# Optimization experiments

Measured on AMD Instinct MI355X. Metric: run time of the kernel, lower is better.

The kernel has to match this reference:

```python
import jax, jax.numpy as jnp
import numpy as np

LN_EPS = 1e-12


def setup_inputs() -> dict:
    key = jax.random.key(0)
    ks = jax.random.split(key, 10)
    B, S, W, D, H = 16, 512, 5, 200, 768
    std = 0.02
    return {
        "layer_output": jax.random.normal(ks[0], (B, S, H), dtype=jnp.float32),
        "word_embeddings": jax.random.normal(ks[1], (B, S, W, D), dtype=jnp.float32),
        "word_mask": jax.random.randint(ks[2], (B, S, W), 0, 2, dtype=jnp.int64),
        "W1": jax.random.normal(ks[3], (D, H), dtype=jnp.float32) * std,
        "b1": jnp.zeros((H,), dtype=jnp.float32),
        "W2": jax.random.normal(ks[4], (H, H), dtype=jnp.float32) * std,
        "b2": jnp.zeros((H,), dtype=jnp.float32),
        "attn_W": jax.random.normal(ks[5], (H, H), dtype=jnp.float32) * std,
        "ln_gamma": jnp.ones((H,), dtype=jnp.float32),
        "ln_beta": jnp.zeros((H,), dtype=jnp.float32),
    }


def reference(layer_output, word_embeddings, word_mask, W1, b1, W2, b2, attn_W, ln_gamma, ln_beta):
    # word_transform: Linear -> Tanh -> Linear (dropout = identity in eval)
    we = jnp.tanh(jnp.einsum("bswd,dh->bswh", word_embeddings, W1) + b1)
    we = jnp.einsum("bswh,hk->bswk", we, W2) + b2  # [B,S,W,H]

    # bilinear word attention: (x @ attn_W) . word_outputs -> score over W
    q = jnp.einsum("bsh,hk->bsk", layer_output, attn_W)  # [B,S,H]
    alpha = jnp.einsum("bsk,bswk->bsw", q, we)            # [B,S,W]
    alpha = alpha + (1.0 - word_mask.astype(alpha.dtype)) * -10000.0
    alpha = jax.nn.softmax(alpha, axis=-1)

    # weighted sum over words + residual
    agg = jnp.einsum("bsw,bswh->bsh", alpha, we)
    h = layer_output + agg

    # LayerNorm (fuse_layer; dropout = identity in eval)
    mu = jnp.mean(h, axis=-1, keepdims=True)
    var = jnp.mean(jnp.square(h - mu), axis=-1, keepdims=True)
    return (h - mu) * jax.lax.rsqrt(var + LN_EPS) * ln_gamma + ln_beta
```

## Files before the change

kernel.cpp:

```cpp
#include <hip/hip_runtime.h>
#include <hip/hip_bf16.h>
#include <math.h>


typedef __attribute__((ext_vector_type(8))) short bf16x8;
typedef __attribute__((ext_vector_type(4))) float f32x4;

__device__ __forceinline__ unsigned short f2bf_bits(float f) {
    __hip_bfloat16 h = __float2bfloat16(f);
    return *reinterpret_cast<unsigned short*>(&h);
}
__device__ __forceinline__ float bf_bits2f(unsigned short u) {
    union { unsigned int i; float f; } v; v.i = ((unsigned int)u) << 16; return v.f;
}
__device__ __forceinline__ float tanh_fast(float x) {
    float xc = fminf(fmaxf(x, -9.f), 9.f);
    float t  = __expf(2.f * xc);
    return (t - 1.f) * __builtin_amdgcn_rcpf(t + 1.f);
}
__device__ __forceinline__ bf16x8 pack8(float4 a, float4 b) {
    union { bf16x8 v; unsigned short s[8]; } u;
    u.s[0]=f2bf_bits(a.x); u.s[1]=f2bf_bits(a.y); u.s[2]=f2bf_bits(a.z); u.s[3]=f2bf_bits(a.w);
    u.s[4]=f2bf_bits(b.x); u.s[5]=f2bf_bits(b.y); u.s[6]=f2bf_bits(b.z); u.s[7]=f2bf_bits(b.w);
    return u.v;
}

__device__ __forceinline__ void async_cp16(const void* g, void* lds) {
#if __has_builtin(__builtin_amdgcn_global_load_lds)
    auto gp = (const __attribute__((address_space(1))) unsigned int*)g;
    auto lp = (__attribute__((address_space(3))) unsigned int*)lds;
    __builtin_amdgcn_global_load_lds(gp, lp, 16, 0, 0);
#else
    *(uint4*)lds = *(const uint4*)g;
#endif
}

__device__ __forceinline__ void sched_fence()  { asm volatile("" ::: "memory"); }
__device__ __forceinline__ void wait8_barrier(){ asm volatile("s_waitcnt vmcnt(8)\ns_barrier" ::: "memory"); }
__device__ __forceinline__ void wait0_barrier(){ asm volatile("s_waitcnt vmcnt(0)\ns_barrier" ::: "memory"); }
__device__ __forceinline__ void barrier_only() { asm volatile("s_barrier" ::: "memory"); }

template<bool F32SRC, bool SINGLE, bool HAS_BIAS, bool TANH_ACT, bool RESID, bool OUT_BF16,
         int N, int K, int KREAL>
__device__ __forceinline__ void gemm_body(
    const void* __restrict__ Ap, const void* __restrict__ Btp,
    const float* __restrict__ bias, const float* __restrict__ resid,
    void* __restrict__ outp, int m0, int n0, unsigned char* smem)
{
    constexpr int NIT = K / 64;
    const int tid  = threadIdx.x;
    const int lane = tid & 63;
    const int wave = tid >> 6;
    const int wm   = wave & 1;
    const int wn   = wave >> 1;
    const int row16 = lane & 15;
    const int kq    = lane >> 4;

    f32x4 acc[4][4];
#pragma unroll
    for (int i = 0; i < 4; i++)
#pragma unroll
        for (int j = 0; j < 4; j++) acc[i][j] = (f32x4){0.f, 0.f, 0.f, 0.f};

    auto compute_tile = [&](const unsigned short* As, const unsigned short* Bs, bool full) {
        bf16x8 af[2][4], bg[2][4];
#pragma unroll
        for (int mi = 0; mi < 4; mi++) {
            const int r = wm * 64 + mi * 16 + row16;
            af[0][mi] = *(const bf16x8*)&As[r * 64 + (kq ^ (r & 7)) * 8];
            if (full) af[1][mi] = *(const bf16x8*)&As[r * 64 + ((4 + kq) ^ (r & 7)) * 8];
        }
#pragma unroll
        for (int ni = 0; ni < 4; ni++) {
            const int r = wn * 64 + ni * 16 + row16;
            bg[0][ni] = *(const bf16x8*)&Bs[r * 64 + (kq ^ (r & 7)) * 8];
            if (full) bg[1][ni] = *(const bf16x8*)&Bs[r * 64 + ((4 + kq) ^ (r & 7)) * 8];
        }
        __builtin_amdgcn_s_setprio(1);
#pragma unroll
        for (int mi = 0; mi < 4; mi++)
#pragma unroll
            for (int ni = 0; ni < 4; ni++)
                acc[mi][ni] = __builtin_amdgcn_mfma_f32_16x16x32_bf16(
                    af[0][mi], bg[0][ni], acc[mi][ni], 0, 0, 0);
        if (full) {
#pragma unroll
            for (int mi = 0; mi < 4; mi++)
#pragma unroll
                for (int ni = 0; ni < 4; ni++)
                    acc[mi][ni] = __builtin_amdgcn_mfma_f32_16x16x32_bf16(
                        af[1][mi], bg[1][ni], acc[mi][ni], 0, 0, 0);
        }
        __builtin_amdgcn_s_setprio(0);
    };

    if constexpr (F32SRC) {
        const float* A32 = (const float*)Ap;
        const float* B32 = (const float*)Btp;
        unsigned short* As = (unsigned short*)smem;
        unsigned short* Bs = As + 8192;
        for (int t = 0; t < NIT; ++t) {
#pragma unroll
            for (int i = 0; i < 4; ++i) {
                const int c = i * 256 + tid;
                const int row = c >> 3, sl = c & 7;
                const int kcc = sl ^ (row & 7);
                const float* sa = A32 + (size_t)(m0 + row) * K + t * 64 + kcc * 8;
                *(bf16x8*)&As[row * 64 + sl * 8] = pack8(*(const float4*)sa, *(const float4*)(sa + 4));
                const float* sb = B32 + (size_t)(n0 + row) * K + t * 64 + kcc * 8;
                *(bf16x8*)&Bs[row * 64 + sl * 8] = pack8(*(const float4*)sb, *(const float4*)(sb + 4));
            }
            __syncthreads();
            compute_tile(As, Bs, true);
            __syncthreads();
        }
    } else {
        const __hip_bfloat16* A  = (const __hip_bfloat16*)Ap;
        const __hip_bfloat16* Bt = (const __hip_bfloat16*)Btp;
        const int rsub = lane >> 3;
        const int slot = lane & 7;
        const int kc   = slot ^ rsub;
        const __hip_bfloat16* gA = A  + (size_t)(m0 + wave * 32 + rsub) * K + kc * 8;
        const __hip_bfloat16* gB = Bt + (size_t)(n0 + wave * 32 + rsub) * K + kc * 8;
        unsigned short* lA0 = (unsigned short*)smem + wave * 2048 + lane * 8;
        unsigned short* lB0 = lA0 + 8192;

        auto stage = [&](int t, int buf) {
            unsigned short* lA = lA0 + buf * 16384;
            unsigned short* lB = lB0 + buf * 16384;
            const __hip_bfloat16* a = gA + t * 64;
            const __hip_bfloat16* b = gB + t * 64;
#pragma unroll
            for (int i = 0; i < 4; i++) {
                async_cp16(a + (size_t)(8 * i) * K, lA + i * 512);
                async_cp16(b + (size_t)(8 * i) * K, lB + i * 512);
            }
            sched_fence();
        };

        if constexpr (SINGLE) {
            static_assert(!SINGLE || NIT <= 4, "SINGLE path needs K<=256 (128KB LDS)");
#pragma unroll
            for (int t = 0; t < NIT; ++t) stage(t, t);
            wait0_barrier();
#pragma unroll
            for (int t = 0; t < NIT; ++t) {
                const unsigned short* As = (const unsigned short*)(smem + t * 32768);
                compute_tile(As, As + 8192, (t * 64 + 32 < KREAL));
            }
            barrier_only();
        } else {
            stage(0, 0);
            if (NIT > 1) stage(1, 1);
#pragma unroll
            for (int t = 0; t < NIT; ++t) {
                if (t == NIT - 1) wait0_barrier(); else wait8_barrier();
                const unsigned short* As = (const unsigned short*)(smem + (t & 1) * 32768);
                const unsigned short* Bs = As + 8192;
                compute_tile(As, Bs, (t * 64 + 32 < KREAL));
                barrier_only();
                if (t + 2 < NIT) stage(t + 2, t & 1);
            }
        }
    }

    if (OUT_BF16) {
        unsigned short* rep = (unsigned short*)smem;
#pragma unroll
        for (int ni = 0; ni < 4; ni++) {
            const int c = wn * 64 + ni * 16 + row16;
            float bcol = HAS_BIAS ? bias[n0 + c] : 0.f;
#pragma unroll
            for (int mi = 0; mi < 4; mi++)
#pragma unroll
                for (int r = 0; r < 4; r++) {
                    const int rr = wm * 64 + mi * 16 + kq * 4 + r;
                    float v = acc[mi][ni][r];
                    if (HAS_BIAS) v += bcol;
                    if (TANH_ACT) v = tanh_fast(v);
                    rep[rr * 132 + c] = f2bf_bits(v);
                }
        }
        __syncthreads();
#pragma unroll
        for (int p = 0; p < 8; p++) {
            const int lin = p * 256 + tid;
            const int row = lin >> 4;
            const int c8  = lin & 15;
            const unsigned short* s = &rep[row * 132 + c8 * 8];
            union { uint4 u; unsigned long long q[2]; } d;
            d.q[0] = *(const unsigned long long*)(s);
            d.q[1] = *(const unsigned long long*)(s + 4);
            *(uint4*)((__hip_bfloat16*)outp + (size_t)(m0 + row) * N + n0 + c8 * 8) = d.u;
        }
    } else {
        float* rep = (float*)smem;
#pragma unroll
        for (int h = 0; h < 2; h++) {
            if (wm == h) {
#pragma unroll
                for (int ni = 0; ni < 4; ni++) {
                    const int c = wn * 64 + ni * 16 + row16;
                    float bcol = HAS_BIAS ? bias[n0 + c] : 0.f;
#pragma unroll
                    for (int mi = 0; mi < 4; mi++)
#pragma unroll
                        for (int r = 0; r < 4; r++) {
                            const int rr = mi * 16 + kq * 4 + r;
                            float v = acc[mi][ni][r];
                            if (HAS_BIAS) v += bcol;
                            if (TANH_ACT) v = tanh_fast(v);
                            rep[rr * 132 + c] = v;
                        }
                }
            }
            __syncthreads();
#pragma unroll
            for (int p = 0; p < 8; p++) {
                const int lin = p * 256 + tid;
                const int row = lin >> 5;
                const int c4  = lin & 31;
                float4 v = *(const float4*)&rep[row * 132 + c4 * 4];
                const int grow = m0 + h * 64 + row;
                if (RESID) {
                    float4 rv = *(const float4*)&resid[(size_t)grow * N + n0 + c4 * 4];
                    v.x += rv.x; v.y += rv.y; v.z += rv.z; v.w += rv.w;
                }
                *(float4*)((float*)outp + (size_t)grow * N + n0 + c4 * 4) = v;
            }
            __syncthreads();
        }
    }
}

template<bool HAS_BIAS, bool TANH_ACT, bool RESID, bool OUT_BF16, int N, int K, int GX>
__global__ __launch_bounds__(256) void mfma_gemm(
    const __hip_bfloat16* __restrict__ A,
    const __hip_bfloat16* __restrict__ Bt,
    const float* __restrict__ bias,
    const float* __restrict__ resid,
    void* __restrict__ outp)
{
    __shared__ __align__(16) unsigned char smem[65536];
    int bx, by;
    {
        const int total = gridDim.x;
        const int per_xcd = total >> 3;
        if ((total & 7) == 0 && (per_xcd % GX) == 0) {
            int xcd = blockIdx.x & 7, idx = blockIdx.x >> 3;
            int lin = xcd * per_xcd + idx;
            by = lin / GX; bx = lin % GX;
        } else { by = blockIdx.x / GX; bx = blockIdx.x % GX; }
    }
    gemm_body<false, false, HAS_BIAS, TANH_ACT, RESID, OUT_BF16, N, K, K>(
        A, Bt, bias, resid, outp, by * 128, bx * 128, smem);
}

__global__ __launch_bounds__(256) void tgemm_kernel(
    const __hip_bfloat16* __restrict__ Eb,
    const __hip_bfloat16* __restrict__ W1Tb,
    const float* __restrict__ b1,
    __hip_bfloat16* __restrict__ Tb)
{
    __shared__ __align__(16) unsigned char smem[131072];
    const int xcd = blockIdx.x & 7, idx = blockIdx.x >> 3;
    const int lin = xcd * 240 + idx;
    gemm_body<false, true, true, true, false, true, 768, 256, 224>(
        Eb, W1Tb, b1, nullptr, Tb, (lin / 6) * 128, (lin % 6) * 128, smem);
}

__global__ __launch_bounds__(256) void prep_kernel(
    const float* __restrict__ x,  __hip_bfloat16* __restrict__ xb,
    const float* __restrict__ w2,
    const float* __restrict__ aw,
    const float* __restrict__ E,  __hip_bfloat16* __restrict__ Eb,
    const float* __restrict__ W1, __hip_bfloat16* __restrict__ W1Tb,
    __hip_bfloat16* __restrict__ W2Tb,
    __hip_bfloat16* __restrict__ Ctb)
{
    __shared__ __align__(16) unsigned char smem[33792];
    float (*tile)[33] = (float(*)[33])smem;
    const int b = blockIdx.x, tid = threadIdx.x;
    if (b < 6144) {
        long long i = (long long)b * 256 + tid;
        float4 v = ((const float4*)x)[i];
        ((ushort4*)xb)[i] = make_ushort4(f2bf_bits(v.x), f2bf_bits(v.y), f2bf_bits(v.z), f2bf_bits(v.w));
    } else if (b < 16384) {
        const int lane = tid & 63, wave = tid >> 6;
        const long long row = (long long)(b - 6144) * 4 + wave;
        const int k = lane * 4;
        float4 v = make_float4(0.f, 0.f, 0.f, 0.f);
        if (k < 200) v = *(const float4*)&E[row * 200 + k];
        *(ushort4*)&Eb[row * 256 + k] =
            make_ushort4(f2bf_bits(v.x), f2bf_bits(v.y), f2bf_bits(v.z), f2bf_bits(v.w));
    } else if (b < 17152) {
        const float* in; __hip_bfloat16* outb; int R, C, Rpad, t;
        if (b < 16576) { t = b - 16384; in = W1; outb = W1Tb; R = 200; C = 768; Rpad = 256; }
        else           { t = b - 16576; in = w2; outb = W2Tb; R = 768; C = 768; Rpad = 768; }
        const int c0 = (t % 24) * 32, r0 = (t / 24) * 32;
        const int xx = tid & 31, yy = tid >> 5;
#pragma unroll
        for (int i = 0; i < 32; i += 8) {
            int r = r0 + yy + i;
            tile[yy + i][xx] = (r < R) ? in[(size_t)r * C + c0 + xx] : 0.f;
        }
        __syncthreads();
#pragma unroll
        for (int i = 0; i < 32; i += 8)
            outb[(size_t)(c0 + yy + i) * Rpad + r0 + xx] = __float2bfloat16(tile[xx][yy + i]);
    } else {
        const int id = b - 17152;
        gemm_body<true, false, false, false, false, true, 768, 768, 768>(
            w2, aw, nullptr, nullptr, Ctb, (id / 6) * 128, (id % 6) * 128, smem);
    }
}

__global__ __launch_bounds__(256) void attn_kernel(
    const __hip_bfloat16* __restrict__ T,
    const __hip_bfloat16* P,
    const int* __restrict__ mask,
    __hip_bfloat16* S)
{
    const int lane = threadIdx.x & 63;
    const int wave = threadIdx.x >> 6;
    const int r    = blockIdx.x * 4 + wave;
    const int base = lane * 12;

    float pv[12];
    {
        const ushort4* pp = (const ushort4*)((const unsigned short*)P + (size_t)r * 768 + base);
        ushort4 u0 = pp[0], u1 = pp[1], u2 = pp[2];
        unsigned short us[12] = {u0.x,u0.y,u0.z,u0.w, u1.x,u1.y,u1.z,u1.w, u2.x,u2.y,u2.z,u2.w};
#pragma unroll
        for (int j = 0; j < 12; j++) pv[j] = bf_bits2f(us[j]);
    }
    float tv[5][12], part[5];
#pragma unroll
    for (int w = 0; w < 5; w++) {
        const ushort4* tp = (const ushort4*)((const unsigned short*)T + ((size_t)r * 5 + w) * 768 + base);
        ushort4 u0 = tp[0], u1 = tp[1], u2 = tp[2];
        unsigned short us[12] = {u0.x,u0.y,u0.z,u0.w, u1.x,u1.y,u1.z,u1.w, u2.x,u2.y,u2.z,u2.w};
        float s = 0.f;
#pragma unroll
        for (int j = 0; j < 12; j++) { tv[w][j] = bf_bits2f(us[j]); s += tv[w][j] * pv[j]; }
        part[w] = s;
    }
#pragma unroll
    for (int off = 32; off > 0; off >>= 1)
#pragma unroll
        for (int w = 0; w < 5; w++)
            part[w] += __shfl_xor(part[w], off, 64);

    float logit[5], mx = -1e30f;
#pragma unroll
    for (int w = 0; w < 5; w++) {
        float m = (float)mask[(size_t)r * 5 + w];
        logit[w] = part[w] - 10000.0f * (1.0f - m);
        mx = fmaxf(mx, logit[w]);
    }
    float se = 0.f;
#pragma unroll
    for (int w = 0; w < 5; w++) { logit[w] = expf(logit[w] - mx); se += logit[w]; }
    const float inv = 1.0f / se;

    unsigned short os[12];
#pragma unroll
    for (int j = 0; j < 12; j++) {
        float s = 0.f;
#pragma unroll
        for (int w = 0; w < 5; w++) s += logit[w] * tv[w][j];
        os[j] = f2bf_bits(s * inv);
    }
    ushort4* sp = (ushort4*)((unsigned short*)S + (size_t)r * 768 + base);
    sp[0] = make_ushort4(os[0], os[1], os[2],  os[3]);
    sp[1] = make_ushort4(os[4], os[5], os[6],  os[7]);
    sp[2] = make_ushort4(os[8], os[9], os[10], os[11]);
}

__global__ __launch_bounds__(256) void ln_kernel(
    const float* __restrict__ Hbuf, const float* __restrict__ gamma,
    const float* __restrict__ beta, float* __restrict__ out)
{
    const int lane = threadIdx.x & 63;
    const int wave = threadIdx.x >> 6;
    const int r    = blockIdx.x * 4 + wave;
    const float* hr = Hbuf + (size_t)r * 768 + lane * 12;

    float v[12];
    {
        float4 a = *(const float4*)(hr);
        float4 b = *(const float4*)(hr + 4);
        float4 c = *(const float4*)(hr + 8);
        v[0]=a.x; v[1]=a.y; v[2]=a.z; v[3]=a.w;
        v[4]=b.x; v[5]=b.y; v[6]=b.z; v[7]=b.w;
        v[8]=c.x; v[9]=c.y; v[10]=c.z; v[11]=c.w;
    }
    float s = 0.f;
#pragma unroll
    for (int j = 0; j < 12; j++) s += v[j];
#pragma unroll
    for (int off = 32; off > 0; off >>= 1) s += __shfl_xor(s, off, 64);
    const float mu = s * (1.f / 768.f);
    float vs = 0.f;
#pragma unroll
    for (int j = 0; j < 12; j++) { float d = v[j] - mu; vs += d * d; }
#pragma unroll
    for (int off = 32; off > 0; off >>= 1) vs += __shfl_xor(vs, off, 64);
    const float rs = rsqrtf(vs * (1.f / 768.f) + 1e-12f);

    float o[12];
#pragma unroll
    for (int j = 0; j < 12; j++) {
        int h = lane * 12 + j;
        o[j] = (v[j] - mu) * rs * gamma[h] + beta[h];
    }
    float* orow = out + (size_t)r * 768 + lane * 12;
    *(float4*)(orow)     = make_float4(o[0], o[1], o[2],  o[3]);
    *(float4*)(orow + 4) = make_float4(o[4], o[5], o[6],  o[7]);
    *(float4*)(orow + 8) = make_float4(o[8], o[9], o[10], o[11]);
}

extern "C" void kernel_launch(void* const* d_in, const int* in_sizes, int n_in,
                              void* d_out, int out_size, void* d_ws, size_t ws_size,
                              hipStream_t stream)
{
    const float* x      = (const float*)d_in[0];
    const float* E      = (const float*)d_in[1];
    const int*   mask   = (const int*)d_in[2];
    const float* W1     = (const float*)d_in[3];
    const float* b1     = (const float*)d_in[4];
    const float* W2     = (const float*)d_in[5];
    const float* b2     = (const float*)d_in[6];
    const float* attn_W = (const float*)d_in[7];
    const float* gamma  = (const float*)d_in[8];
    const float* beta   = (const float*)d_in[9];
    float* out = (float*)d_out;

    const int BS = 8192, H = 768, M1 = 40960, KP = 256;

    char* p = (char*)d_ws;
    auto alloc = [&](size_t bytes) { char* q = p; p += (bytes + 255) & ~(size_t)255; return q; };
    __hip_bfloat16* xb    = (__hip_bfloat16*)alloc((size_t)BS * H * 2);
    __hip_bfloat16* W2Tb  = (__hip_bfloat16*)alloc((size_t)H * H * 2);
    __hip_bfloat16* Ctb   = (__hip_bfloat16*)alloc((size_t)H * H * 2);
    __hip_bfloat16* W1Tb  = (__hip_bfloat16*)alloc((size_t)H * KP * 2);
    __hip_bfloat16* Tb    = (__hip_bfloat16*)alloc((size_t)M1 * H * 2);
    __hip_bfloat16* Eb    = (__hip_bfloat16*)alloc((size_t)M1 * KP * 2);
    float* Hb = (float*)Tb;
    __hip_bfloat16* Pb = Eb;
    __hip_bfloat16* Sb = Pb;

    prep_kernel<<<17188, 256, 0, stream>>>(x, xb, W2, attn_W, E, Eb, W1, W1Tb, W2Tb, Ctb);

    tgemm_kernel<<<1920, 256, 0, stream>>>(Eb, W1Tb, b1, Tb);

    mfma_gemm<false, false, false, true, 768, 768, 6><<<384, 256, 0, stream>>>(
        xb, Ctb, nullptr, nullptr, Pb);

    attn_kernel<<<BS / 4, 256, 0, stream>>>(Tb, Pb, mask, Sb);

    mfma_gemm<true, false, true, false, 768, 768, 6><<<384, 256, 0, stream>>>(
        Sb, W2Tb, b2, x, Hb);

    ln_kernel<<<BS / 4, 256, 0, stream>>>(Hb, gamma, beta, out);
}
```

Baseline: 252.0 us.

## Double-buffer tgemm with 64KB LDS and coarsen prep kernel blocks

The first GEMM drops its single-shot load of all four K tiles into 128KB of LDS and uses the same two-buffer pipelined loop as the other GEMMs, with 64KB LDS. This is meant to allow higher occupancy and overlap loads with MFMA work. The prep kernel moves its long Ctb GEMM blocks to the front of the grid so they start early. Each conversion block now handles 8x more float4 or row work, which cuts the grid from 17188 to 2852 blocks and lowers per-block overhead, at the cost of less parallelism per block.

```diff
diff --git a/kernel.cpp b/kernel.cpp
--- a/kernel.cpp
+++ b/kernel.cpp
@@ -40,7 +40,7 @@
 __device__ __forceinline__ void wait0_barrier(){ asm volatile("s_waitcnt vmcnt(0)\ns_barrier" ::: "memory"); }
 __device__ __forceinline__ void barrier_only() { asm volatile("s_barrier" ::: "memory"); }
 
-template<bool F32SRC, bool SINGLE, bool HAS_BIAS, bool TANH_ACT, bool RESID, bool OUT_BF16,
+template<bool F32SRC, bool HAS_BIAS, bool TANH_ACT, bool RESID, bool OUT_BF16,
          int N, int K, int KREAL>
 __device__ __forceinline__ void gemm_body(
     const void* __restrict__ Ap, const void* __restrict__ Btp,
@@ -138,29 +138,16 @@
             sched_fence();
         };
 
-        if constexpr (SINGLE) {
-            static_assert(!SINGLE || NIT <= 4, "SINGLE path needs K<=256 (128KB LDS)");
-#pragma unroll
-            for (int t = 0; t < NIT; ++t) stage(t, t);
-            wait0_barrier();
-#pragma unroll
-            for (int t = 0; t < NIT; ++t) {
-                const unsigned short* As = (const unsigned short*)(smem + t * 32768);
-                compute_tile(As, As + 8192, (t * 64 + 32 < KREAL));
-            }
+        stage(0, 0);
+        if (NIT > 1) stage(1, 1);
+#pragma unroll
+        for (int t = 0; t < NIT; ++t) {
+            if (t == NIT - 1) wait0_barrier(); else wait8_barrier();
+            const unsigned short* As = (const unsigned short*)(smem + (t & 1) * 32768);
+            const unsigned short* Bs = As + 8192;
+            compute_tile(As, Bs, (t * 64 + 32 < KREAL));
             barrier_only();
-        } else {
-            stage(0, 0);
-            if (NIT > 1) stage(1, 1);
-#pragma unroll
-            for (int t = 0; t < NIT; ++t) {
-                if (t == NIT - 1) wait0_barrier(); else wait8_barrier();
-                const unsigned short* As = (const unsigned short*)(smem + (t & 1) * 32768);
-                const unsigned short* Bs = As + 8192;
-                compute_tile(As, Bs, (t * 64 + 32 < KREAL));
-                barrier_only();
-                if (t + 2 < NIT) stage(t + 2, t & 1);
-            }
+            if (t + 2 < NIT) stage(t + 2, t & 1);
         }
     }
 
@@ -252,7 +239,7 @@
             by = lin / GX; bx = lin % GX;
         } else { by = blockIdx.x / GX; bx = blockIdx.x % GX; }
     }
-    gemm_body<false, false, HAS_BIAS, TANH_ACT, RESID, OUT_BF16, N, K, K>(
+    gemm_body<false, HAS_BIAS, TANH_ACT, RESID, OUT_BF16, N, K, K>(
         A, Bt, bias, resid, outp, by * 128, bx * 128, smem);
 }
 
@@ -262,10 +249,10 @@
     const float* __restrict__ b1,
     __hip_bfloat16* __restrict__ Tb)
 {
-    __shared__ __align__(16) unsigned char smem[131072];
+    __shared__ __align__(16) unsigned char smem[65536];
     const int xcd = blockIdx.x & 7, idx = blockIdx.x >> 3;
     const int lin = xcd * 240 + idx;
-    gemm_body<false, true, true, true, false, true, 768, 256, 224>(
+    gemm_body<false, true, true, false, true, 768, 256, 224>(
         Eb, W1Tb, b1, nullptr, Tb, (lin / 6) * 128, (lin % 6) * 128, smem);
 }
 
@@ -281,22 +268,13 @@
     __shared__ __align__(16) unsigned char smem[33792];
     float (*tile)[33] = (float(*)[33])smem;
     const int b = blockIdx.x, tid = threadIdx.x;
-    if (b < 6144) {
-        long long i = (long long)b * 256 + tid;
-        float4 v = ((const float4*)x)[i];
-        ((ushort4*)xb)[i] = make_ushort4(f2bf_bits(v.x), f2bf_bits(v.y), f2bf_bits(v.z), f2bf_bits(v.w));
-    } else if (b < 16384) {
-        const int lane = tid & 63, wave = tid >> 6;
-        const long long row = (long long)(b - 6144) * 4 + wave;
-        const int k = lane * 4;
-        float4 v = make_float4(0.f, 0.f, 0.f, 0.f);
-        if (k < 200) v = *(const float4*)&E[row * 200 + k];
-        *(ushort4*)&Eb[row * 256 + k] =
-            make_ushort4(f2bf_bits(v.x), f2bf_bits(v.y), f2bf_bits(v.z), f2bf_bits(v.w));
-    } else if (b < 17152) {
+    if (b < 36) {
+        gemm_body<true, false, false, false, true, 768, 768, 768>(
+            w2, aw, nullptr, nullptr, Ctb, (b / 6) * 128, (b % 6) * 128, smem);
+    } else if (b < 804) {
         const float* in; __hip_bfloat16* outb; int R, C, Rpad, t;
-        if (b < 16576) { t = b - 16384; in = W1; outb = W1Tb; R = 200; C = 768; Rpad = 256; }
-        else           { t = b - 16576; in = w2; outb = W2Tb; R = 768; C = 768; Rpad = 768; }
+        if (b < 228) { t = b - 36;  in = W1; outb = W1Tb; R = 200; C = 768; Rpad = 256; }
+        else         { t = b - 228; in = w2; outb = W2Tb; R = 768; C = 768; Rpad = 768; }
         const int c0 = (t % 24) * 32, r0 = (t / 24) * 32;
         const int xx = tid & 31, yy = tid >> 5;
 #pragma unroll
@@ -308,10 +286,29 @@
 #pragma unroll
         for (int i = 0; i < 32; i += 8)
             outb[(size_t)(c0 + yy + i) * Rpad + r0 + xx] = __float2bfloat16(tile[xx][yy + i]);
+    } else if (b < 1572) {
+        const long long base = (long long)(b - 804) * 2048 + tid;
+        float4 v[8];
+#pragma unroll
+        for (int j = 0; j < 8; j++) v[j] = ((const float4*)x)[base + j * 256];
+#pragma unroll
+        for (int j = 0; j < 8; j++)
+            ((ushort4*)xb)[base + j * 256] =
+                make_ushort4(f2bf_bits(v[j].x), f2bf_bits(v[j].y), f2bf_bits(v[j].z), f2bf_bits(v[j].w));
     } else {
-        const int id = b - 17152;
-        gemm_body<true, false, false, false, false, true, 768, 768, 768>(
-            w2, aw, nullptr, nullptr, Ctb, (id / 6) * 128, (id % 6) * 128, smem);
+        const int lane = tid & 63, wave = tid >> 6;
+        const long long r0 = (long long)(b - 1572) * 32 + wave * 8;
+        const int k = lane * 4;
+        float4 v[8];
+#pragma unroll
+        for (int j = 0; j < 8; j++) {
+            v[j] = make_float4(0.f, 0.f, 0.f, 0.f);
+            if (k < 200) v[j] = *(const float4*)&E[(r0 + j) * 200 + k];
+        }
+#pragma unroll
+        for (int j = 0; j < 8; j++)
+            *(ushort4*)&Eb[(r0 + j) * 256 + k] =
+                make_ushort4(f2bf_bits(v[j].x), f2bf_bits(v[j].y), f2bf_bits(v[j].z), f2bf_bits(v[j].w));
     }
 }
 
@@ -450,7 +447,7 @@
     __hip_bfloat16* Pb = Eb;
     __hip_bfloat16* Sb = Pb;
 
-    prep_kernel<<<17188, 256, 0, stream>>>(x, xb, W2, attn_W, E, Eb, W1, W1Tb, W2Tb, Ctb);
+    prep_kernel<<<2852, 256, 0, stream>>>(x, xb, W2, attn_W, E, Eb, W1, W1Tb, W2Tb, Ctb);
 
     tgemm_kernel<<<1920, 256, 0, stream>>>(Eb, W1Tb, b1, Tb);
 
```

New measurement: 217.3 us. 1.16x faster.
